# Kernel optimization log

Measured on AMD Instinct MI355X. Metric: run time of the kernel, lower is better.

Reference implementation:

```python
import jax, jax.numpy as jnp
import numpy as np

GROUP = 64
DIM = 4096
N_HEADS = 32
N_KV = 8
HEAD_DIM = DIM // N_HEADS  # 128
N_REP = N_HEADS // N_KV    # 4
B = 1
S = 2048
THETA = 1e6


def _pack_q40(rng, out_f, in_f):
    """Random int4 weights packed Q4_0 style (two nibbles per int8) + per-group scales."""
    q = rng.integers(-7, 8, size=(out_f * in_f,)).reshape(-1, 2, GROUP)
    packed = ((q[:, 0] << 4) | (q[:, 1] & 15)).astype(np.int8)  # [out*in/group/2, group]
    scale = (np.abs(rng.standard_normal((out_f * in_f // GROUP, 1))) * 0.01 + 1e-3).astype(np.float32)
    return jnp.asarray(packed), jnp.asarray(scale)


def dequantize_q40(w, scale, shape):
    """Faithful port of torch dequantize_q40: arithmetic shifts sign-extend nibbles."""
    msb = jnp.right_shift(w, 4)                          # high nibble, sign-extended
    lsb = jnp.right_shift(jnp.left_shift(w, 4), 4)       # low nibble, sign-extended
    grp = jnp.concatenate([msb, lsb], axis=1).reshape(-1, GROUP)  # hstack then view(-1, group)
    return (grp.astype(scale.dtype) * scale).reshape(shape)


def setup_inputs() -> dict:
    rng = np.random.default_rng(0)
    wq, sq = _pack_q40(rng, N_HEADS * HEAD_DIM, DIM)
    wk, sk = _pack_q40(rng, N_KV * HEAD_DIM, DIM)
    wv, sv = _pack_q40(rng, N_KV * HEAD_DIM, DIM)
    wo, so = _pack_q40(rng, DIM, N_HEADS * HEAD_DIM)
    x = jnp.asarray(rng.standard_normal((B, S, DIM)), jnp.float32)
    inv_freq = 1.0 / (THETA ** (np.arange(0, HEAD_DIM, 2, dtype=np.float64) / HEAD_DIM))
    ang = np.outer(np.arange(S, dtype=np.float64), inv_freq)  # [S, HEAD_DIM/2]
    cos = jnp.asarray(np.cos(ang), jnp.float32)
    sin = jnp.asarray(np.sin(ang), jnp.float32)
    causal = np.triu(np.ones((S, S), dtype=bool), k=1)
    mask = jnp.asarray(np.where(causal, -1e9, 0.0), jnp.float32)
    return dict(x=x, wq=wq, sq=sq, wk=wk, sk=sk, wv=wv, sv=sv, wo=wo, so=so,
                cos=cos, sin=sin, mask=mask)


def _rotate_half(t):
    h = t.shape[-1] // 2
    return jnp.concatenate([-t[..., h:], t[..., :h]], axis=-1)


def reference(x, wq, sq, wk, sk, wv, sv, wo, so, cos, sin, mask):
    # Dequant-then-matmul QKV projections (weights stored as [out, in])
    Wq = dequantize_q40(wq, sq, (N_HEADS * HEAD_DIM, DIM))
    Wk = dequantize_q40(wk, sk, (N_KV * HEAD_DIM, DIM))
    Wv = dequantize_q40(wv, sv, (N_KV * HEAD_DIM, DIM))
    Wo = dequantize_q40(wo, so, (DIM, N_HEADS * HEAD_DIM))

    xq = (x @ Wq.T).reshape(B, S, N_HEADS, HEAD_DIM)
    xk = (x @ Wk.T).reshape(B, S, N_KV, HEAD_DIM)
    xv = (x @ Wv.T).reshape(B, S, N_KV, HEAD_DIM)

    # RoPE (rotate-half convention): cos/sin are [S, HEAD_DIM/2] -> cat to [S, HEAD_DIM]
    cosf = jnp.concatenate([cos, cos], axis=-1)[:, None, :]  # [S, 1, HEAD_DIM]
    sinf = jnp.concatenate([sin, sin], axis=-1)[:, None, :]
    xq = xq * cosf + _rotate_half(xq) * sinf
    xk = xk * cosf + _rotate_half(xk) * sinf

    # start_pos == 0 prefill: keys/values are the freshly projected xk/xv
    # GQA: repeat_interleave over the kv-head dim
    keys = jnp.repeat(xk, N_REP, axis=2)    # [B, S, N_HEADS, HEAD_DIM]
    values = jnp.repeat(xv, N_REP, axis=2)

    scores = jnp.einsum('bqhd,bkhd->bhqk', xq, keys) / np.float32(np.sqrt(HEAD_DIM))
    scores = scores + mask  # additive causal mask broadcast over [B, H]
    attn = jax.nn.softmax(scores, axis=-1)
    out = jnp.einsum('bhqk,bkhd->bqhd', attn, values).reshape(B, S, N_HEADS * HEAD_DIM)
    return out @ Wo.T
```

## Files before the change

kernel.cpp:

```cpp
#include <hip/hip_runtime.h>
#include <stdint.h>

#define DIMX 4096
#define NH   32
#define NKV  8
#define HD   128
#define SEQ  2048
#define QKVD 6144

typedef _Float16 h16;
typedef __attribute__((ext_vector_type(8))) _Float16 h16x8;
typedef __attribute__((ext_vector_type(4))) _Float16 h16x4;
typedef __attribute__((ext_vector_type(4))) float   f32x4;

__device__ __forceinline__ void gload_lds16(const void* g, void* l) {
  __builtin_amdgcn_global_load_lds(
      (const __attribute__((address_space(1))) void*)g,
      (__attribute__((address_space(3))) void*)l, 16, 0, 0);
}

template <int CTRL>
__device__ __forceinline__ float dpp_mv(float x) {
  int y = __builtin_amdgcn_mov_dpp(__builtin_bit_cast(int, x), CTRL, 0xF, 0xF, true);
  return __builtin_bit_cast(float, y);
}
__device__ __forceinline__ float red16_max(float x) {
  x = fmaxf(x, dpp_mv<0xB1>(x));
  x = fmaxf(x, dpp_mv<0x1B>(x));
  x = fmaxf(x, dpp_mv<0x141>(x));
  x = fmaxf(x, dpp_mv<0x140>(x));
  return x;
}
__device__ __forceinline__ float red16_sum(float x) {
  x += dpp_mv<0xB1>(x);
  x += dpp_mv<0x1B>(x);
  x += dpp_mv<0x141>(x);
  x += dpp_mv<0x140>(x);
  return x;
}

template <int PERM>
__device__ __forceinline__ void dq_unit(const void* __restrict__ w, const float* __restrict__ sc,
                                        h16* __restrict__ out, int u, int flag) {
  uint32_t b4;
  if (flag) {
    const int4 t = *(const int4*)((const int*)w + 4 * u);
    b4 = (uint32_t)(t.x & 0xFF) | ((uint32_t)(t.y & 0xFF) << 8) |
         ((uint32_t)(t.z & 0xFF) << 16) | ((uint32_t)(t.w & 0xFF) << 24);
  } else {
    b4 = ((const uint32_t*)w)[u];
  }
  int r = u >> 4;
  int p = (u & 15) * 4;
  float shi = sc[2 * r], slo = sc[2 * r + 1];
  h16x4 hi, lo;
#pragma unroll
  for (int j = 0; j < 4; ++j) {
    int by = (int)((b4 >> (8 * j)) & 0xFF);
    int hn = (by << 24) >> 28;
    int ln = (by << 28) >> 28;
    hi[j] = (h16)((float)hn * shi);
    lo[j] = (h16)((float)ln * slo);
  }
  size_t base;
  if (PERM) {
    int row  = r >> 5;
    int rowp = (row & ~127) | (((row & 63) << 1) | ((row >> 6) & 1));
    base = ((size_t)rowp << 12) + (size_t)((r & 31) << 7);
  } else {
    base = (size_t)r << 7;
  }
  *(h16x4*)(out + base + p)      = hi;
  *(h16x4*)(out + base + 64 + p) = lo;
}

#define U_WQ 2097152
#define U_WK 524288
#define U_WV 524288
#define U_WO 2097152

__global__ __launch_bounds__(256) void prep_all(
    const void* __restrict__ wq, const float* __restrict__ sq,
    const void* __restrict__ wk, const float* __restrict__ sk,
    const void* __restrict__ wv, const float* __restrict__ sv,
    const void* __restrict__ wo, const float* __restrict__ so,
    const float4* __restrict__ x,
    h16* __restrict__ Wqkv, h16* __restrict__ Wo, h16x4* __restrict__ xb) {
  __shared__ int sfl;
  if (threadIdx.x == 0) {
    int ok = 1;
    const int* wi = (const int*)wq;
    for (int i = 0; i < 64; ++i) {
      int v = wi[i];
      if (v < -128 || v > 127) ok = 0;
    }
    sfl = ok;
  }
  __syncthreads();
  const int fl = sfl;
  int u = blockIdx.x * 256 + threadIdx.x;
  if (u < U_WQ) { dq_unit<1>(wq, sq, Wqkv, u, fl); return; }
  u -= U_WQ;
  if (u < U_WK) { dq_unit<1>(wk, sk, Wqkv + 16777216, u, fl); return; }
  u -= U_WK;
  if (u < U_WV) { dq_unit<0>(wv, sv, Wqkv + 20971520, u, fl); return; }
  u -= U_WV;
  if (u < U_WO) { dq_unit<0>(wo, so, Wo, u, fl); return; }
  u -= U_WO;
  {
    float4 v = x[u];
    h16x4 o;
    o.x = (h16)v.x; o.y = (h16)v.y; o.z = (h16)v.z; o.w = (h16)v.w;
    xb[u] = o;
  }
}

template <typename OutT, int NT, int MODE>
__global__ __launch_bounds__(512, 2) void gemm_pipe(
    const h16* __restrict__ A, const h16* __restrict__ B, OutT* __restrict__ C,
    int N, int K,
    const float* __restrict__ cosb, const float* __restrict__ sinb,
    h16* __restrict__ vt) {
  constexpr int NSLOT = 4 + NT;
  constexpr int BUFH  = NSLOT * 4096;
  __shared__ __attribute__((aligned(16))) h16 SM[2 * BUFH];

  const int tid  = threadIdx.x;
  const int w    = tid >> 6, lane = tid & 63;
  const int wr   = w >> 1, wc = w & 1;
  const int quad = lane >> 4, l15 = lane & 15;
  const int axr  = l15 & 7;
  const int m0 = blockIdx.y * 256, n0 = blockIdx.x * (NT * 64);

  const h16* Ab = A + (size_t)m0 * K;
  const h16* Bb = B + (size_t)n0 * K;
  const int srow = tid >> 3;
  const int sg8  = ((tid & 7) ^ (srow & 7)) * 8;

  f32x4 acc[2][2][2][NT];
#pragma unroll
  for (int a = 0; a < 2; ++a)
#pragma unroll
    for (int b = 0; b < 2; ++b)
#pragma unroll
      for (int mt = 0; mt < 2; ++mt)
#pragma unroll
        for (int nt = 0; nt < NT; ++nt) acc[a][b][mt][nt] = (f32x4){0.f, 0.f, 0.f, 0.f};

  h16x8 af[2][2][2];
  h16x8 bf1[NT][2];
  h16x8 bf0E[NT][2], bf0O[NT][2];

#define STG(sl_, tile_) do {                                                        \
    const h16* g_ = ((sl_) < 4) ? (Ab + (size_t)((sl_) * 64) * K)                   \
                                : (Bb + (size_t)(((sl_) - 4) * 64) * K);            \
    char* d_ = (char*)(SM + ((tile_) & 1) * BUFH + (sl_) * 4096);                   \
    gload_lds16(g_ + (size_t)srow * K + (tile_) * 64 + sg8, d_ + tid * 16);         \
  } while (0)

#define LDA_(tile_, a_) do {                                                        \
    const h16* s_ = SM + ((tile_) & 1) * BUFH + wr * 4096;                          \
    _Pragma("unroll") for (int mt = 0; mt < 2; ++mt)                                \
    _Pragma("unroll") for (int ks = 0; ks < 2; ++ks)                                \
      af[a_][mt][ks] = *(const h16x8*)&s_[((a_) * 32 + mt * 16 + l15) * 64 +        \
                                          (((ks * 4 + quad) ^ axr) * 8)];           \
  } while (0)

#define LDB1_(tile_) do {                                                           \
    const h16* s_ = SM + ((tile_) & 1) * BUFH + 16384;                              \
    _Pragma("unroll") for (int nt = 0; nt < NT; ++nt)                               \
    _Pragma("unroll") for (int ks = 0; ks < 2; ++ks)                                \
      bf1[nt][ks] = *(const h16x8*)&s_[(NT * 32 + wc * (NT * 16) + nt * 16 + l15) * 64 + \
                                       (((ks * 4 + quad) ^ axr) * 8)];              \
  } while (0)

#define LDB0_(tile_, D_) do {                                                       \
    const h16* s_ = SM + ((tile_) & 1) * BUFH + 16384;                              \
    _Pragma("unroll") for (int nt = 0; nt < NT; ++nt)                               \
    _Pragma("unroll") for (int ks = 0; ks < 2; ++ks)                                \
      D_[nt][ks] = *(const h16x8*)&s_[(wc * (NT * 16) + nt * 16 + l15) * 64 +       \
                                      (((ks * 4 + quad) ^ axr) * 8)];               \
  } while (0)

#define MMAB1(a_) do {                                                              \
    __builtin_amdgcn_s_setprio(1);                                                  \
    _Pragma("unroll") for (int mt = 0; mt < 2; ++mt)                                \
    _Pragma("unroll") for (int nt = 0; nt < NT; ++nt)                               \
    _Pragma("unroll") for (int ks = 0; ks < 2; ++ks)                                \
      acc[a_][1][mt][nt] = __builtin_amdgcn_mfma_f32_16x16x32_f16(                  \
          af[a_][mt][ks], bf1[nt][ks], acc[a_][1][mt][nt], 0, 0, 0);                \
    __builtin_amdgcn_s_setprio(0);                                                  \
  } while (0)

#define MMAB0(a_, D_) do {                                                          \
    __builtin_amdgcn_s_setprio(1);                                                  \
    _Pragma("unroll") for (int mt = 0; mt < 2; ++mt)                                \
    _Pragma("unroll") for (int nt = 0; nt < NT; ++nt)                               \
    _Pragma("unroll") for (int ks = 0; ks < 2; ++ks)                                \
      acc[a_][0][mt][nt] = __builtin_amdgcn_mfma_f32_16x16x32_f16(                  \
          af[a_][mt][ks], D_[nt][ks], acc[a_][0][mt][nt], 0, 0, 0);                 \
    __builtin_amdgcn_s_setprio(0);                                                  \
  } while (0)

#define CFENCE asm volatile("" ::: "memory")
#define BARX do { CFENCE; __builtin_amdgcn_s_barrier(); CFENCE; } while (0)
#define W2 do { if constexpr (NT == 3) asm volatile("s_waitcnt vmcnt(7)" ::: "memory"); \
                else                   asm volatile("s_waitcnt vmcnt(6)" ::: "memory"); } while (0)
#define W3 do { if constexpr (NT == 3) asm volatile("s_waitcnt vmcnt(3)" ::: "memory"); \
                else                   asm volatile("s_waitcnt vmcnt(2)" ::: "memory"); } while (0)
#define VM0  asm volatile("s_waitcnt vmcnt(0)" ::: "memory")

  const int NTILE = K >> 6;
  const int NIT   = K >> 7;

  STG(4, 0); STG(5, 0);
  if constexpr (NT == 3) STG(6, 0);
  STG(0, 0); STG(1, 0); STG(2, 0); STG(3, 0);
  STG(4, 1); STG(5, 1);
  if constexpr (NT == 3) STG(6, 1);
  STG(0, 1); STG(1, 1); STG(2, 1); STG(3, 1);
  W2;
  BARX;
  LDA_(0, 0); LDB0_(0, bf0E);

  for (int i = 0; i < NIT; ++i) {
    const int t0 = 2 * i, t1 = 2 * i + 1;
    const int T2 = (t0 + 2 < NTILE) ? t0 + 2 : NTILE - 1;
    const int T3 = (t1 + 2 < NTILE) ? t1 + 2 : NTILE - 1;
    LDB1_(t0);
    MMAB0(0, bf0E); BARX;
    LDA_(t0, 1); STG(4, T2); W2;
    MMAB1(0); BARX;
    LDB0_(t1, bf0O); STG(5, T2);
    if constexpr (NT == 3) STG(6, T2);
    W3;
    MMAB1(1); BARX;
    LDA_(t1, 0); STG(0, T2); STG(1, T2); STG(2, T2); STG(3, T2);
    MMAB0(1, bf0E); BARX;
    LDB1_(t1);
    MMAB0(0, bf0O); BARX;
    LDA_(t1, 1); STG(4, T3); W2;
    MMAB1(0); BARX;
    LDB0_(T2, bf0E); STG(5, T3);
    if constexpr (NT == 3) STG(6, T3);
    W3;
    MMAB1(1); BARX;
    LDA_(T2, 0); STG(0, T3); STG(1, T3); STG(2, T3); STG(3, T3);
    MMAB0(1, bf0O); BARX;
  }
  VM0;

  if constexpr (MODE == 1) {
#pragma unroll
    for (int a = 0; a < 2; ++a)
#pragma unroll
      for (int b = 0; b < 2; ++b)
#pragma unroll
        for (int mt = 0; mt < 2; ++mt)
#pragma unroll
          for (int nt = 0; nt < NT; ++nt) {
            const int cb   = n0 + b * (NT * 32) + wc * (NT * 16) + nt * 16;
            const int row0 = m0 + wr * 64 + a * 32 + mt * 16 + quad * 4;
            if (cb >= 5120) {
              const int dcol = cb + l15 - 5120;
              h16x4 vvv;
#pragma unroll
              for (int r = 0; r < 4; ++r) vvv[r] = (h16)acc[a][b][mt][nt][r];
              *(h16x4*)(vt + (size_t)dcol * SEQ + row0) = vvv;
            } else {
              const float qs = (cb < 4096) ? 0.08838834764831845f : 1.0f;
              const int col = cb + l15;
              const int j   = (col & 127) >> 1;
              const float sgn = (col & 1) ? 1.f : -1.f;
#pragma unroll
              for (int r = 0; r < 4; ++r) {
                float own = acc[a][b][mt][nt][r];
                float par = dpp_mv<0xB1>(own);
                float cc  = cosb[(size_t)(row0 + r) * 64 + j];
                float ss  = sinb[(size_t)(row0 + r) * 64 + j];
                C[(size_t)(row0 + r) * N + col] = (OutT)((own * cc + sgn * par * ss) * qs);
              }
            }
          }
  } else {
#pragma unroll
    for (int a = 0; a < 2; ++a)
#pragma unroll
      for (int b = 0; b < 2; ++b)
#pragma unroll
        for (int mt = 0; mt < 2; ++mt)
#pragma unroll
          for (int nt = 0; nt < NT; ++nt)
#pragma unroll
            for (int r = 0; r < 4; ++r) {
              int row = m0 + wr * 64 + a * 32 + mt * 16 + quad * 4 + r;
              int col = n0 + b * (NT * 32) + wc * (NT * 16) + nt * 16 + l15;
              C[(size_t)row * N + col] = (OutT)acc[a][b][mt][nt][r];
            }
  }
#undef STG
#undef LDA_
#undef LDB1_
#undef LDB0_
#undef MMAB1
#undef MMAB0
#undef CFENCE
#undef BARX
#undef W2
#undef W3
#undef VM0
}

__global__ __launch_bounds__(256, 2) void flash_attn(
    const h16* __restrict__ qkv, const h16* __restrict__ vt, h16* __restrict__ o_out) {
  __shared__ __attribute__((aligned(16))) h16 Ks[64 * 128];
  __shared__ __attribute__((aligned(16))) h16 Vts[128 * 64];
  __shared__ __attribute__((aligned(16))) h16 Ps[4][32 * 72];

  const int tid  = threadIdx.x;
  const int w    = tid >> 6, lane = tid & 63;
  const int quad = lane >> 4, l15 = lane & 15;
  const int h    = blockIdx.x;
  const int y    = blockIdx.y;
  const int qt   = (y < 8) ? (15 - y) : (y - 8);
  const int kv   = h >> 2;
  const int rowq = qt * 128 + w * 32;
  const h16* vtg = vt + (size_t)kv * HD * SEQ;

  h16x8 qf[2][4];
#pragma unroll
  for (int mt = 0; mt < 2; ++mt) {
    const h16* qrow = qkv + (size_t)(rowq + mt * 16 + l15) * QKVD + h * 128;
#pragma unroll
    for (int ks = 0; ks < 4; ++ks)
      qf[mt][ks] = *(const h16x8*)(qrow + ks * 32 + quad * 8);
  }

  f32x4 o[2][8];
#pragma unroll
  for (int mt = 0; mt < 2; ++mt)
#pragma unroll
    for (int i = 0; i < 8; ++i) o[mt][i] = (f32x4){0.f, 0.f, 0.f, 0.f};
  float mrow[2][4], lrow[2][4];
#pragma unroll
  for (int mt = 0; mt < 2; ++mt)
#pragma unroll
    for (int r = 0; r < 4; ++r) { mrow[mt][r] = -3e30f; lrow[mt][r] = 0.f; }
  h16* Psw = Ps[w];

  h16x8 kreg[4], vreg[4];
#define LOADT(k0_) do {                                                              \
    _Pragma("unroll") for (int i = 0; i < 4; ++i) {                                  \
      int c = i * 256 + tid; int key = c >> 4, d8s = c & 15;                         \
      kreg[i] = *(const h16x8*)(qkv + (size_t)((k0_) + key) * QKVD + 4096 +          \
                                kv * 128 + ((d8s ^ (key & 15)) * 8));                \
    }                                                                                \
    _Pragma("unroll") for (int i = 0; i < 4; ++i) {                                  \
      int c = i * 256 + tid; int d = c >> 3, p = c & 7;                              \
      vreg[i] = *(const h16x8*)(vtg + (size_t)d * SEQ + (k0_) + ((p ^ (d & 7)) * 8));\
    }                                                                                \
  } while (0)

  const int nkt = 2 * qt + 2;
  LOADT(0);
  for (int kt = 0; kt < nkt; ++kt) {
    const int k0 = kt * 64;
    __syncthreads();
#pragma unroll
    for (int i = 0; i < 4; ++i) *(h16x8*)((char*)Ks + (i * 256 + tid) * 16) = kreg[i];
#pragma unroll
    for (int i = 0; i < 4; ++i) *(h16x8*)((char*)Vts + (i * 256 + tid) * 16) = vreg[i];
    __syncthreads();
    const int knx = (kt + 1 < nkt) ? (kt + 1) * 64 : k0;
    LOADT(knx);

    if (k0 <= rowq + 31) {
      float alpha[2][4];
      f32x4 s2[2][4];
#pragma unroll
      for (int nt = 0; nt < 4; ++nt) {
        int key = nt * 16 + l15;
        f32x4 a0 = (f32x4){0.f, 0.f, 0.f, 0.f};
        f32x4 a1 = (f32x4){0.f, 0.f, 0.f, 0.f};
#pragma unroll
        for (int ks = 0; ks < 4; ++ks) {
          int d8 = ks * 4 + quad;
          h16x8 kf = *(const h16x8*)&Ks[key * 128 + ((d8 ^ (key & 15)) * 8)];
          a0 = __builtin_amdgcn_mfma_f32_16x16x32_f16(qf[0][ks], kf, a0, 0, 0, 0);
          a1 = __builtin_amdgcn_mfma_f32_16x16x32_f16(qf[1][ks], kf, a1, 0, 0, 0);
        }
        s2[0][nt] = a0;
        s2[1][nt] = a1;
      }
      const bool needmask = (k0 + 63 > rowq);
      float tm2[2][4];
      float need = -3e30f;
#pragma unroll
      for (int mt = 0; mt < 2; ++mt) {
#pragma unroll
        for (int r = 0; r < 4; ++r) {
          float tm = -3e30f;
          if (needmask) {
            int rowg = rowq + mt * 16 + quad * 4 + r;
#pragma unroll
            for (int nt = 0; nt < 4; ++nt) {
              float v = s2[mt][nt][r];
              if (k0 + nt * 16 + l15 > rowg) v = -3e30f;
              s2[mt][nt][r] = v;
              tm = fmaxf(tm, v);
            }
          } else {
#pragma unroll
            for (int nt = 0; nt < 4; ++nt) tm = fmaxf(tm, s2[mt][nt][r]);
          }
          tm = red16_max(tm);
          tm2[mt][r] = tm;
          need = fmaxf(need, tm - mrow[mt][r]);
        }
      }
      if (__any(need > 8.0f)) {
#pragma unroll
        for (int mt = 0; mt < 2; ++mt)
#pragma unroll
          for (int r = 0; r < 4; ++r) {
            float mnew = fmaxf(mrow[mt][r], tm2[mt][r]);
            alpha[mt][r] = __expf(mrow[mt][r] - mnew);
            mrow[mt][r] = mnew;
          }
#pragma unroll
        for (int mt = 0; mt < 2; ++mt)
#pragma unroll
          for (int on = 0; on < 8; ++on) {
            o[mt][on][0] *= alpha[mt][0]; o[mt][on][1] *= alpha[mt][1];
            o[mt][on][2] *= alpha[mt][2]; o[mt][on][3] *= alpha[mt][3];
          }
#pragma unroll
        for (int mt = 0; mt < 2; ++mt)
#pragma unroll
          for (int r = 0; r < 4; ++r) lrow[mt][r] *= alpha[mt][r];
      }
#pragma unroll
      for (int mt = 0; mt < 2; ++mt) {
#pragma unroll
        for (int r = 0; r < 4; ++r) {
          float m = mrow[mt][r];
          float ps = 0.f;
#pragma unroll
          for (int nt = 0; nt < 4; ++nt) {
            float e = __expf(s2[mt][nt][r] - m);
            ps += e;
            Psw[(mt * 16 + quad * 4 + r) * 72 + nt * 16 + l15] = (h16)e;
          }
          ps = red16_sum(ps);
          lrow[mt][r] += ps;
        }
      }
      asm volatile("s_waitcnt lgkmcnt(0)" ::: "memory");
#pragma unroll
      for (int ks = 0; ks < 2; ++ks) {
        h16x8 pf0 = *(const h16x8*)&Psw[(0  + l15) * 72 + ks * 32 + quad * 8];
        h16x8 pf1 = *(const h16x8*)&Psw[(16 + l15) * 72 + ks * 32 + quad * 8];
        int k8 = ks * 4 + quad;
#pragma unroll
        for (int on = 0; on < 8; ++on) {
          int d = on * 16 + l15;
          h16x8 vf = *(const h16x8*)&Vts[d * 64 + ((k8 ^ (d & 7)) * 8)];
          o[0][on] = __builtin_amdgcn_mfma_f32_16x16x32_f16(pf0, vf, o[0][on], 0, 0, 0);
          o[1][on] = __builtin_amdgcn_mfma_f32_16x16x32_f16(pf1, vf, o[1][on], 0, 0, 0);
        }
      }
    }
  }
#undef LOADT
#pragma unroll
  for (int mt = 0; mt < 2; ++mt) {
    float linv[4];
#pragma unroll
    for (int r = 0; r < 4; ++r) linv[r] = 1.0f / lrow[mt][r];
#pragma unroll
    for (int on = 0; on < 8; ++on)
#pragma unroll
      for (int r = 0; r < 4; ++r) {
        int row = rowq + mt * 16 + quad * 4 + r;
        int col = h * 128 + on * 16 + l15;
        o_out[(size_t)row * DIMX + col] = (h16)(o[mt][on][r] * linv[r]);
      }
  }
}

extern "C" void kernel_launch(void* const* d_in, const int* in_sizes, int n_in,
                              void* d_out, int out_size, void* d_ws, size_t ws_size,
                              hipStream_t stream) {
  const float* x    = (const float*)d_in[0];
  const void*  wq   = d_in[1];
  const float* sq   = (const float*)d_in[2];
  const void*  wk   = d_in[3];
  const float* sk   = (const float*)d_in[4];
  const void*  wv   = d_in[5];
  const float* sv   = (const float*)d_in[6];
  const void*  wo   = d_in[7];
  const float* so   = (const float*)d_in[8];
  const float* cosb = (const float*)d_in[9];
  const float* sinb = (const float*)d_in[10];
  float* out = (float*)d_out;

  char* ws = (char*)d_ws;
  h16* Wqkv = (h16*)ws;
  h16* Wo   = (h16*)(ws + 50331648);
  h16* xb   = (h16*)(ws + 83886080);
  h16* qkv  = (h16*)(ws + 100663296);
  h16* vt   = (h16*)d_out;

  prep_all<<<28672, 256, 0, stream>>>(wq, sq, wk, sk, wv, sv, wo, so,
                                      (const float4*)x, Wqkv, Wo, (h16x4*)xb);

  gemm_pipe<h16, 3, 1><<<dim3(32, 8), 512, 0, stream>>>(
      xb, Wqkv, qkv, QKVD, DIMX, cosb, sinb, vt);

  flash_attn<<<dim3(32, 16), 256, 0, stream>>>(qkv, vt, xb);

  gemm_pipe<float, 2, 0><<<dim3(32, 8), 512, 0, stream>>>(
      xb, Wo, out, DIMX, DIMX, cosb, sinb, vt);
}
```

Measured before the change: 415.1 us.

## Restructure GEMM pipeline into four phases and remap block indices

The GEMM main loop drops from eight barrier-separated MFMA phases per iteration to four. It loads both A halves and the B fragments together, then issues the A-tile stages for the next tile before a larger MFMA batch. The prologue and wait counts change to match the new staging order. Blocks are also remapped from a linearized index: in the GEMM, consecutive blocks walk M tiles first (hardcoded 8x32 grid), and in attention, consecutive blocks go to different KV groups. This is meant to cut barrier overhead and improve cache and XCD locality, but it adds hazard risk from the changed vmcnt accounting and hardcodes the grid shape.

```diff
diff --git a/kernel.cpp b/kernel.cpp
--- a/kernel.cpp
+++ b/kernel.cpp
@@ -130,7 +130,10 @@
   const int wr   = w >> 1, wc = w & 1;
   const int quad = lane >> 4, l15 = lane & 15;
   const int axr  = l15 & 7;
-  const int m0 = blockIdx.y * 256, n0 = blockIdx.x * (NT * 64);
+  const int hlin = (int)(blockIdx.y * gridDim.x + blockIdx.x);
+  const int lby  = hlin & 7;
+  const int lbx  = (hlin >> 3) & 31;
+  const int m0 = lby * 256, n0 = lbx * (NT * 64);
 
   const h16* Ab = A + (size_t)m0 * K;
   const h16* Bb = B + (size_t)n0 * K;
@@ -204,49 +207,45 @@
 
 #define CFENCE asm volatile("" ::: "memory")
 #define BARX do { CFENCE; __builtin_amdgcn_s_barrier(); CFENCE; } while (0)
-#define W2 do { if constexpr (NT == 3) asm volatile("s_waitcnt vmcnt(7)" ::: "memory"); \
-                else                   asm volatile("s_waitcnt vmcnt(6)" ::: "memory"); } while (0)
-#define W3 do { if constexpr (NT == 3) asm volatile("s_waitcnt vmcnt(3)" ::: "memory"); \
+#define WA   asm volatile("s_waitcnt vmcnt(4)" ::: "memory")
+#define WB do { if constexpr (NT == 3) asm volatile("s_waitcnt vmcnt(3)" ::: "memory"); \
                 else                   asm volatile("s_waitcnt vmcnt(2)" ::: "memory"); } while (0)
 #define VM0  asm volatile("s_waitcnt vmcnt(0)" ::: "memory")
 
   const int NTILE = K >> 6;
   const int NIT   = K >> 7;
 
+  STG(0, 0); STG(1, 0); STG(2, 0); STG(3, 0);
   STG(4, 0); STG(5, 0);
   if constexpr (NT == 3) STG(6, 0);
-  STG(0, 0); STG(1, 0); STG(2, 0); STG(3, 0);
   STG(4, 1); STG(5, 1);
   if constexpr (NT == 3) STG(6, 1);
-  STG(0, 1); STG(1, 1); STG(2, 1); STG(3, 1);
-  W2;
+  WB;
   BARX;
-  LDA_(0, 0); LDB0_(0, bf0E);
+  LDB0_(0, bf0E);
 
   for (int i = 0; i < NIT; ++i) {
     const int t0 = 2 * i, t1 = 2 * i + 1;
     const int T2 = (t0 + 2 < NTILE) ? t0 + 2 : NTILE - 1;
     const int T3 = (t1 + 2 < NTILE) ? t1 + 2 : NTILE - 1;
-    LDB1_(t0);
-    MMAB0(0, bf0E); BARX;
-    LDA_(t0, 1); STG(4, T2); W2;
-    MMAB1(0); BARX;
-    LDB0_(t1, bf0O); STG(5, T2);
+    LDA_(t0, 0); LDA_(t0, 1); LDB1_(t0);
+    STG(0, t1); STG(1, t1); STG(2, t1); STG(3, t1);
+    MMAB0(0, bf0E); MMAB1(0);
+    WA; BARX;
+    LDB0_(t1, bf0O);
+    STG(4, T2); STG(5, T2);
     if constexpr (NT == 3) STG(6, T2);
-    W3;
-    MMAB1(1); BARX;
-    LDA_(t1, 0); STG(0, T2); STG(1, T2); STG(2, T2); STG(3, T2);
-    MMAB0(1, bf0E); BARX;
-    LDB1_(t1);
-    MMAB0(0, bf0O); BARX;
-    LDA_(t1, 1); STG(4, T3); W2;
-    MMAB1(0); BARX;
-    LDB0_(T2, bf0E); STG(5, T3);
+    MMAB1(1); MMAB0(1, bf0E);
+    WB; BARX;
+    LDA_(t1, 0); LDA_(t1, 1); LDB1_(t1);
+    STG(0, T2); STG(1, T2); STG(2, T2); STG(3, T2);
+    MMAB0(0, bf0O); MMAB1(0);
+    WA; BARX;
+    LDB0_(T2, bf0E);
+    STG(4, T3); STG(5, T3);
     if constexpr (NT == 3) STG(6, T3);
-    W3;
-    MMAB1(1); BARX;
-    LDA_(T2, 0); STG(0, T3); STG(1, T3); STG(2, T3); STG(3, T3);
-    MMAB0(1, bf0O); BARX;
+    MMAB1(1); MMAB0(1, bf0O);
+    WB; BARX;
   }
   VM0;
 
@@ -306,8 +305,8 @@
 #undef MMAB0
 #undef CFENCE
 #undef BARX
-#undef W2
-#undef W3
+#undef WA
+#undef WB
 #undef VM0
 }
 
@@ -320,7 +319,8 @@
   const int tid  = threadIdx.x;
   const int w    = tid >> 6, lane = tid & 63;
   const int quad = lane >> 4, l15 = lane & 15;
-  const int h    = blockIdx.x;
+  const int hp   = blockIdx.x;
+  const int h    = ((hp & 7) << 2) | (hp >> 3);
   const int y    = blockIdx.y;
   const int qt   = (y < 8) ? (15 - y) : (y - 8);
   const int kv   = h >> 2;
```

New measurement: 425.5 us. 2.5% more time.

## Restructure GEMM pipeline with triple-buffered B slabs and split-N MFMA phases

Applied to the files above, without the earlier changes.

Reworks the LDS staging of the pipelined fp16 GEMM. A stays double-buffered, while B is split into a B0 slab and a B1 slab that are each triple-buffered and prefetched one or more tiles ahead. Each k-tile now runs two MFMA phases, one per B slab, over the full 128-row warp A fragment, and the A fragments alternate between even and odd register sets. The aim is to cut barriers per tile and hide more global-to-LDS latency. The cost is more LDS, a different register footprint, and hand-tuned vmcnt waits that could be wrong, which would give a race.

```diff
diff --git a/kernel.cpp b/kernel.cpp
--- a/kernel.cpp
+++ b/kernel.cpp
@@ -121,9 +121,13 @@
     int N, int K,
     const float* __restrict__ cosb, const float* __restrict__ sinb,
     h16* __restrict__ vt) {
-  constexpr int NSLOT = 4 + NT;
-  constexpr int BUFH  = NSLOT * 4096;
-  __shared__ __attribute__((aligned(16))) h16 SM[2 * BUFH];
+  constexpr int B0SZ   = (NT == 3) ? 8192 : 4096;
+  constexpr int B0ROWS = (NT == 3) ? 128 : 64;
+  constexpr int NB0    = (NT == 3) ? 4 : 2;
+  constexpr int B0BASE = 32768;
+  constexpr int B1BASE = 32768 + 3 * B0SZ;
+  constexpr int SMSZ   = B1BASE + 3 * 4096;
+  __shared__ __attribute__((aligned(16))) h16 SM[SMSZ];
 
   const int tid  = threadIdx.x;
   const int w    = tid >> 6, lane = tid & 63;
@@ -137,177 +141,202 @@
   const int srow = tid >> 3;
   const int sg8  = ((tid & 7) ^ (srow & 7)) * 8;
 
-  f32x4 acc[2][2][2][NT];
+  f32x4 acc0[2][2][NB0];
+  f32x4 acc1[2][2][2];
 #pragma unroll
   for (int a = 0; a < 2; ++a)
 #pragma unroll
-    for (int b = 0; b < 2; ++b)
-#pragma unroll
-      for (int mt = 0; mt < 2; ++mt)
-#pragma unroll
-        for (int nt = 0; nt < NT; ++nt) acc[a][b][mt][nt] = (f32x4){0.f, 0.f, 0.f, 0.f};
-
-  h16x8 af[2][2][2];
-  h16x8 bf1[NT][2];
-  h16x8 bf0E[NT][2], bf0O[NT][2];
-
-#define STG(sl_, tile_) do {                                                        \
-    const h16* g_ = ((sl_) < 4) ? (Ab + (size_t)((sl_) * 64) * K)                   \
-                                : (Bb + (size_t)(((sl_) - 4) * 64) * K);            \
-    char* d_ = (char*)(SM + ((tile_) & 1) * BUFH + (sl_) * 4096);                   \
-    gload_lds16(g_ + (size_t)srow * K + (tile_) * 64 + sg8, d_ + tid * 16);         \
-  } while (0)
-
-#define LDA_(tile_, a_) do {                                                        \
-    const h16* s_ = SM + ((tile_) & 1) * BUFH + wr * 4096;                          \
+    for (int mt = 0; mt < 2; ++mt) {
+#pragma unroll
+      for (int nt = 0; nt < NB0; ++nt) acc0[a][mt][nt] = (f32x4){0.f, 0.f, 0.f, 0.f};
+#pragma unroll
+      for (int nt = 0; nt < 2; ++nt)   acc1[a][mt][nt] = (f32x4){0.f, 0.f, 0.f, 0.f};
+    }
+
+  h16x8 afE[2][2][2], afO[2][2][2];
+  h16x8 bf0[NB0][2];
+  h16x8 bf1[2][2];
+
+#define STGA(sl_, tile_) gload_lds16(                                               \
+    Ab + (size_t)((sl_) * 64 + srow) * K + (tile_) * 64 + sg8,                      \
+    (char*)(SM + ((tile_) & 1) * 16384 + (sl_) * 4096) + tid * 16)
+#define STGB0(sl_, tile_) gload_lds16(                                              \
+    Bb + (size_t)((sl_) * 64 + srow) * K + (tile_) * 64 + sg8,                      \
+    (char*)(SM + B0BASE + ((tile_) % 3) * B0SZ + (sl_) * 4096) + tid * 16)
+#define STGB1(tile_) gload_lds16(                                                   \
+    Bb + (size_t)(B0ROWS + srow) * K + (tile_) * 64 + sg8,                          \
+    (char*)(SM + B1BASE + ((tile_) % 3) * 4096) + tid * 16)
+
+#define LDAF(tile_, D_) do {                                                        \
+    const h16* s_ = SM + ((tile_) & 1) * 16384;                                     \
+    _Pragma("unroll") for (int a = 0; a < 2; ++a)                                   \
     _Pragma("unroll") for (int mt = 0; mt < 2; ++mt)                                \
     _Pragma("unroll") for (int ks = 0; ks < 2; ++ks)                                \
-      af[a_][mt][ks] = *(const h16x8*)&s_[((a_) * 32 + mt * 16 + l15) * 64 +        \
-                                          (((ks * 4 + quad) ^ axr) * 8)];           \
+      D_[a][mt][ks] = *(const h16x8*)&s_[(wr * 64 + a * 32 + mt * 16 + l15) * 64 +  \
+                                         (((ks * 4 + quad) ^ axr) * 8)];            \
+  } while (0)
+
+#define LDB0_(tile_) do {                                                           \
+    const h16* s_ = SM + B0BASE + ((tile_) % 3) * B0SZ;                             \
+    _Pragma("unroll") for (int nt = 0; nt < NB0; ++nt)                              \
+    _Pragma("unroll") for (int ks = 0; ks < 2; ++ks)                                \
+      bf0[nt][ks] = *(const h16x8*)&s_[(wc * (B0ROWS / 2) + nt * 16 + l15) * 64 +   \
+                                       (((ks * 4 + quad) ^ axr) * 8)];              \
   } while (0)
 
 #define LDB1_(tile_) do {                                                           \
-    const h16* s_ = SM + ((tile_) & 1) * BUFH + 16384;                              \
-    _Pragma("unroll") for (int nt = 0; nt < NT; ++nt)                               \
+    const h16* s_ = SM + B1BASE + ((tile_) % 3) * 4096;                             \
+    _Pragma("unroll") for (int nt = 0; nt < 2; ++nt)                                \
     _Pragma("unroll") for (int ks = 0; ks < 2; ++ks)                                \
-      bf1[nt][ks] = *(const h16x8*)&s_[(NT * 32 + wc * (NT * 16) + nt * 16 + l15) * 64 + \
+      bf1[nt][ks] = *(const h16x8*)&s_[(wc * 32 + nt * 16 + l15) * 64 +             \
                                        (((ks * 4 + quad) ^ axr) * 8)];              \
   } while (0)
 
-#define LDB0_(tile_, D_) do {                                                       \
-    const h16* s_ = SM + ((tile_) & 1) * BUFH + 16384;                              \
-    _Pragma("unroll") for (int nt = 0; nt < NT; ++nt)                               \
+#define MMA0(AF_) do {                                                              \
+    __builtin_amdgcn_s_setprio(1);                                                  \
+    _Pragma("unroll") for (int a = 0; a < 2; ++a)                                   \
+    _Pragma("unroll") for (int mt = 0; mt < 2; ++mt)                                \
+    _Pragma("unroll") for (int nt = 0; nt < NB0; ++nt)                              \
     _Pragma("unroll") for (int ks = 0; ks < 2; ++ks)                                \
-      D_[nt][ks] = *(const h16x8*)&s_[(wc * (NT * 16) + nt * 16 + l15) * 64 +       \
-                                      (((ks * 4 + quad) ^ axr) * 8)];               \
-  } while (0)
-
-#define MMAB1(a_) do {                                                              \
+      acc0[a][mt][nt] = __builtin_amdgcn_mfma_f32_16x16x32_f16(                     \
+          AF_[a][mt][ks], bf0[nt][ks], acc0[a][mt][nt], 0, 0, 0);                   \
+    __builtin_amdgcn_s_setprio(0);                                                  \
+  } while (0)
+
+#define MMA1(AF_) do {                                                              \
     __builtin_amdgcn_s_setprio(1);                                                  \
+    _Pragma("unroll") for (int a = 0; a < 2; ++a)                                   \
     _Pragma("unroll") for (int mt = 0; mt < 2; ++mt)                                \
-    _Pragma("unroll") for (int nt = 0; nt < NT; ++nt)                               \
+    _Pragma("unroll") for (int nt = 0; nt < 2; ++nt)                                \
     _Pragma("unroll") for (int ks = 0; ks < 2; ++ks)                                \
-      acc[a_][1][mt][nt] = __builtin_amdgcn_mfma_f32_16x16x32_f16(                  \
-          af[a_][mt][ks], bf1[nt][ks], acc[a_][1][mt][nt], 0, 0, 0);                \
-    __builtin_amdgcn_s_setprio(0);                                                  \
-  } while (0)
-
-#define MMAB0(a_, D_) do {                                                          \
-    __builtin_amdgcn_s_setprio(1);                                                  \
-    _Pragma("unroll") for (int mt = 0; mt < 2; ++mt)                                \
-    _Pragma("unroll") for (int nt = 0; nt < NT; ++nt)                               \
-    _Pragma("unroll") for (int ks = 0; ks < 2; ++ks)                                \
-      acc[a_][0][mt][nt] = __builtin_amdgcn_mfma_f32_16x16x32_f16(                  \
-          af[a_][mt][ks], D_[nt][ks], acc[a_][0][mt][nt], 0, 0, 0);                 \
+      acc1[a][mt][nt] = __builtin_amdgcn_mfma_f32_16x16x32_f16(                     \
+          AF_[a][mt][ks], bf1[nt][ks], acc1[a][mt][nt], 0, 0, 0);                   \
     __builtin_amdgcn_s_setprio(0);                                                  \
   } while (0)
 
 #define CFENCE asm volatile("" ::: "memory")
 #define BARX do { CFENCE; __builtin_amdgcn_s_barrier(); CFENCE; } while (0)
-#define W2 do { if constexpr (NT == 3) asm volatile("s_waitcnt vmcnt(7)" ::: "memory"); \
-                else                   asm volatile("s_waitcnt vmcnt(6)" ::: "memory"); } while (0)
-#define W3 do { if constexpr (NT == 3) asm volatile("s_waitcnt vmcnt(3)" ::: "memory"); \
-                else                   asm volatile("s_waitcnt vmcnt(2)" ::: "memory"); } while (0)
+#define WPRE do { if constexpr (NT == 3) asm volatile("s_waitcnt vmcnt(6)" ::: "memory"); \
+                  else                   asm volatile("s_waitcnt vmcnt(5)" ::: "memory"); } while (0)
+#define WPA  do { if constexpr (NT == 3) asm volatile("s_waitcnt vmcnt(3)" ::: "memory"); \
+                  else                   asm volatile("s_waitcnt vmcnt(2)" ::: "memory"); } while (0)
+#define WPB  do { if constexpr (NT == 3) asm volatile("s_waitcnt vmcnt(7)" ::: "memory"); \
+                  else                   asm volatile("s_waitcnt vmcnt(6)" ::: "memory"); } while (0)
 #define VM0  asm volatile("s_waitcnt vmcnt(0)" ::: "memory")
-
-  const int NTILE = K >> 6;
-  const int NIT   = K >> 7;
-
-  STG(4, 0); STG(5, 0);
-  if constexpr (NT == 3) STG(6, 0);
-  STG(0, 0); STG(1, 0); STG(2, 0); STG(3, 0);
-  STG(4, 1); STG(5, 1);
-  if constexpr (NT == 3) STG(6, 1);
-  STG(0, 1); STG(1, 1); STG(2, 1); STG(3, 1);
-  W2;
+#define STGB0ALL(tile_) do { STGB0(0, tile_); if constexpr (NT == 3) STGB0(1, tile_); } while (0)
+#define STGAALL(tile_)  do { STGA(0, tile_); STGA(1, tile_); STGA(2, tile_); STGA(3, tile_); } while (0)
+
+  const int L = (K >> 6) - 1;
+
+  STGAALL(0);
+  STGB0ALL(0); STGB0ALL(1);
+  STGB1(0); STGB1(1);
+  STGAALL(1);
+  STGB0ALL(2);
+  WPRE;
   BARX;
-  LDA_(0, 0); LDB0_(0, bf0E);
-
+  LDAF(0, afE);
+  LDB0_(0);
+
+  const int NIT = (K >> 6) >> 1;
   for (int i = 0; i < NIT; ++i) {
     const int t0 = 2 * i, t1 = 2 * i + 1;
-    const int T2 = (t0 + 2 < NTILE) ? t0 + 2 : NTILE - 1;
-    const int T3 = (t1 + 2 < NTILE) ? t1 + 2 : NTILE - 1;
+    const int t0p2 = (t0 + 2 < L) ? t0 + 2 : L;
+    const int t0p3 = (t0 + 3 < L) ? t0 + 3 : L;
+    const int t1p1 = (t1 + 1 < L) ? t1 + 1 : L;
+    const int t1p2 = (t1 + 2 < L) ? t1 + 2 : L;
+    const int t1p3 = (t1 + 3 < L) ? t1 + 3 : L;
     LDB1_(t0);
-    MMAB0(0, bf0E); BARX;
-    LDA_(t0, 1); STG(4, T2); W2;
-    MMAB1(0); BARX;
-    LDB0_(t1, bf0O); STG(5, T2);
-    if constexpr (NT == 3) STG(6, T2);
-    W3;
-    MMAB1(1); BARX;
-    LDA_(t1, 0); STG(0, T2); STG(1, T2); STG(2, T2); STG(3, T2);
-    MMAB0(1, bf0E); BARX;
+    MMA0(afE);
+    LDB0_(t0 + 1);
+    STGB1(t0p2);
+    WPA; BARX;
+    LDAF(t1, afO);
+    MMA1(afE);
+    STGAALL(t0p2); STGB0ALL(t0p3);
+    WPB; BARX;
     LDB1_(t1);
-    MMAB0(0, bf0O); BARX;
-    LDA_(t1, 1); STG(4, T3); W2;
-    MMAB1(0); BARX;
-    LDB0_(T2, bf0E); STG(5, T3);
-    if constexpr (NT == 3) STG(6, T3);
-    W3;
-    MMAB1(1); BARX;
-    LDA_(T2, 0); STG(0, T3); STG(1, T3); STG(2, T3); STG(3, T3);
-    MMAB0(1, bf0O); BARX;
+    MMA0(afO);
+    LDB0_(t1p1);
+    STGB1(t1p2);
+    WPA; BARX;
+    LDAF(t1p1, afE);
+    MMA1(afO);
+    STGAALL(t1p2); STGB0ALL(t1p3);
+    WPB; BARX;
   }
   VM0;
 
   if constexpr (MODE == 1) {
+#define EPI1(ACC_, CB_) do {                                                        \
+    const int cb   = (CB_);                                                         \
+    const int row0 = m0 + wr * 64 + a * 32 + mt * 16 + quad * 4;                    \
+    if (cb >= 5120) {                                                               \
+      const int dcol = cb + l15 - 5120;                                             \
+      h16x4 vvv;                                                                    \
+      _Pragma("unroll") for (int r = 0; r < 4; ++r) vvv[r] = (h16)ACC_[r];          \
+      *(h16x4*)(vt + (size_t)dcol * SEQ + row0) = vvv;                              \
+    } else {                                                                        \
+      const float qs = (cb < 4096) ? 0.08838834764831845f : 1.0f;                   \
+      const int col = cb + l15;                                                     \
+      const int j   = (col & 127) >> 1;                                             \
+      const float sgn = (col & 1) ? 1.f : -1.f;                                     \
+      _Pragma("unroll") for (int r = 0; r < 4; ++r) {                               \
+        float own = ACC_[r];                                                        \
+        float par = dpp_mv<0xB1>(own);                                              \
+        float cc  = cosb[(size_t)(row0 + r) * 64 + j];                              \
+        float ss  = sinb[(size_t)(row0 + r) * 64 + j];                              \
+        C[(size_t)(row0 + r) * N + col] = (OutT)((own * cc + sgn * par * ss) * qs); \
+      }                                                                             \
+    }                                                                               \
+  } while (0)
 #pragma unroll
     for (int a = 0; a < 2; ++a)
 #pragma unroll
-      for (int b = 0; b < 2; ++b)
-#pragma unroll
-        for (int mt = 0; mt < 2; ++mt)
-#pragma unroll
-          for (int nt = 0; nt < NT; ++nt) {
-            const int cb   = n0 + b * (NT * 32) + wc * (NT * 16) + nt * 16;
-            const int row0 = m0 + wr * 64 + a * 32 + mt * 16 + quad * 4;
-            if (cb >= 5120) {
-              const int dcol = cb + l15 - 5120;
-              h16x4 vvv;
-#pragma unroll
-              for (int r = 0; r < 4; ++r) vvv[r] = (h16)acc[a][b][mt][nt][r];
-              *(h16x4*)(vt + (size_t)dcol * SEQ + row0) = vvv;
-            } else {
-              const float qs = (cb < 4096) ? 0.08838834764831845f : 1.0f;
-              const int col = cb + l15;
-              const int j   = (col & 127) >> 1;
-              const float sgn = (col & 1) ? 1.f : -1.f;
-#pragma unroll
-              for (int r = 0; r < 4; ++r) {
-                float own = acc[a][b][mt][nt][r];
-                float par = dpp_mv<0xB1>(own);
-                float cc  = cosb[(size_t)(row0 + r) * 64 + j];
-                float ss  = sinb[(size_t)(row0 + r) * 64 + j];
-                C[(size_t)(row0 + r) * N + col] = (OutT)((own * cc + sgn * par * ss) * qs);
-              }
-            }
-          }
+      for (int mt = 0; mt < 2; ++mt) {
+#pragma unroll
+        for (int nt = 0; nt < NB0; ++nt)
+          EPI1(acc0[a][mt][nt], n0 + wc * (B0ROWS / 2) + nt * 16);
+#pragma unroll
+        for (int nt = 0; nt < 2; ++nt)
+          EPI1(acc1[a][mt][nt], n0 + B0ROWS + wc * 32 + nt * 16);
+      }
+#undef EPI1
   } else {
 #pragma unroll
     for (int a = 0; a < 2; ++a)
 #pragma unroll
-      for (int b = 0; b < 2; ++b)
-#pragma unroll
-        for (int mt = 0; mt < 2; ++mt)
-#pragma unroll
-          for (int nt = 0; nt < NT; ++nt)
-#pragma unroll
-            for (int r = 0; r < 4; ++r) {
-              int row = m0 + wr * 64 + a * 32 + mt * 16 + quad * 4 + r;
-              int col = n0 + b * (NT * 32) + wc * (NT * 16) + nt * 16 + l15;
-              C[(size_t)row * N + col] = (OutT)acc[a][b][mt][nt][r];
-            }
-  }
-#undef STG
-#undef LDA_
+      for (int mt = 0; mt < 2; ++mt) {
+        const int row0 = m0 + wr * 64 + a * 32 + mt * 16 + quad * 4;
+#pragma unroll
+        for (int nt = 0; nt < NB0; ++nt)
+#pragma unroll
+          for (int r = 0; r < 4; ++r)
+            C[(size_t)(row0 + r) * N + n0 + wc * (B0ROWS / 2) + nt * 16 + l15] =
+                (OutT)acc0[a][mt][nt][r];
+#pragma unroll
+        for (int nt = 0; nt < 2; ++nt)
+#pragma unroll
+          for (int r = 0; r < 4; ++r)
+            C[(size_t)(row0 + r) * N + n0 + B0ROWS + wc * 32 + nt * 16 + l15] =
+                (OutT)acc1[a][mt][nt][r];
+      }
+  }
+#undef STGA
+#undef STGB0
+#undef STGB1
+#undef STGB0ALL
+#undef STGAALL
+#undef LDAF
+#undef LDB0_
 #undef LDB1_
-#undef LDB0_
-#undef MMAB1
-#undef MMAB0
+#undef MMA0
+#undef MMA1
 #undef CFENCE
 #undef BARX
-#undef W2
-#undef W3
+#undef WPRE
+#undef WPA
+#undef WPB
 #undef VM0
 }
 
```

Result: no change. 414.0 us (-0.3%).
